# Optimization experiments

Hardware: AMD Instinct MI355X
Metric: run time of the kernel (lower is better)

Reference implementation:

```python
import jax, jax.numpy as jnp
import numpy as np


def _quant8(w):
    # Brevitas Int8 per-tensor weight quant: scale = max|w|/127, round, clip, dequant.
    s = jnp.max(jnp.abs(w)) / 127.0
    q = jnp.clip(jnp.round(w / s), -127.0, 127.0) * s
    # straight-through estimator (matches brevitas backward)
    return w + jax.lax.stop_gradient(q - w)


def _conv1d(x, w, b):
    # x: [B, Cin, L], w: [Cout, Cin, K]
    y = jax.lax.conv_general_dilated(x, w, window_strides=(1,), padding='VALID',
                                     dimension_numbers=('NCW', 'OIW', 'NCW'))
    return y + b[None, :, None]


def _maxpool2(x):
    B, C, L = x.shape
    L2 = L // 2
    return jnp.max(x[:, :, :2 * L2].reshape(B, C, L2, 2), axis=-1)


def _lrelu(x):
    return jnp.where(x > 0, x, 0.1 * x)


def setup_inputs() -> dict:
    key = jax.random.key(0)
    ks = jax.random.split(key, 13)
    B, C, L = 32768, 2, 128
    flat = 32 * 27  # 864, from tracing conv/pool stack at L=128
    d = {
        'x': jax.random.normal(ks[0], (B, C, L), dtype=jnp.float32),
        'w1': jax.random.normal(ks[1], (16, 2, 2), dtype=jnp.float32) * 0.3,
        'b1': jax.random.normal(ks[2], (16,), dtype=jnp.float32) * 0.05,
        'w2': jax.random.normal(ks[3], (16, 16, 3), dtype=jnp.float32) * 0.1,
        'b2': jax.random.normal(ks[4], (16,), dtype=jnp.float32) * 0.05,
        'w3': jax.random.normal(ks[5], (32, 16, 5), dtype=jnp.float32) * 0.1,
        'b3': jax.random.normal(ks[6], (32,), dtype=jnp.float32) * 0.05,
        'w4': jax.random.normal(ks[7], (32, 32, 5), dtype=jnp.float32) * 0.08,
        'b4': jax.random.normal(ks[8], (32,), dtype=jnp.float32) * 0.05,
        'wd': jax.random.normal(ks[9], (64, flat), dtype=jnp.float32) * 0.03,
        'bd': jax.random.normal(ks[10], (64,), dtype=jnp.float32) * 0.05,
        'wo': jax.random.normal(ks[11], (1, 64), dtype=jnp.float32) * 0.1,
        'bo': jax.random.normal(ks[12], (1,), dtype=jnp.float32) * 0.05,
    }
    return d


def reference(x, w1, b1, w2, b2, w3, b3, w4, b4, wd, bd, wo, bo):
    h = _lrelu(_conv1d(x, _quant8(w1), b1))        # [B,16,127]
    h = _lrelu(_conv1d(h, _quant8(w2), b2))        # [B,16,125]
    h = _maxpool2(h)                               # [B,16,62]
    h = _lrelu(_conv1d(h, _quant8(w3), b3))        # [B,32,58]
    h = _lrelu(_conv1d(h, _quant8(w4), b4))        # [B,32,54]
    h = _maxpool2(h)                               # [B,32,27]
    h = h.reshape(h.shape[0], -1)                  # [B,864]
    h = _lrelu(h @ _quant8(wd).T + bd)             # [B,64]
    return h @ _quant8(wo).T + bo                  # [B,1]
```

## Files before the change

### kernel.cpp

```cpp
#include <hip/hip_runtime.h>
#include <hip/hip_bf16.h>

typedef __hip_bfloat16 bf16;
typedef _Float16 h16;
typedef __attribute__((ext_vector_type(8))) _Float16 h16x8;
typedef __attribute__((ext_vector_type(4))) float f32x4;
typedef __attribute__((ext_vector_type(16))) float f32x16;

__device__ __forceinline__ float lrelu(float x) { return fmaxf(x, 0.1f * x); }
__device__ __forceinline__ float ldE(const void* p, long i, int f32) {
    return f32 ? ((const float*)p)[i] : __bfloat162float(((const bf16*)p)[i]);
}
__device__ __forceinline__ uint2 pack4(float a, float b, float c, float d) {
    union { _Float16 h[4]; uint2 u; } t;
    t.h[0] = (_Float16)a; t.h[1] = (_Float16)b; t.h[2] = (_Float16)c; t.h[3] = (_Float16)d;
    return t.u;
}
__device__ __forceinline__ unsigned umx(unsigned a, unsigned b) { return a > b ? a : b; }
#define LDS_FENCE() asm volatile("s_waitcnt lgkmcnt(0)" ::: "memory")


__device__ __forceinline__ float qv(const void* src, int idx, float sc, int f32) {
    float w = ldE(src, idx, f32);
    float q = rintf(w / sc);
    return fminf(127.f, fmaxf(-127.f, q)) * sc;
}

__device__ float block_scale(const void* src, int n, int f32, int tid, float* red) {
    unsigned m = 0;
    const uint4* p = (const uint4*)src;
    if (f32) {
        int nv = n >> 2;
        for (int i = tid; i < nv; i += 256) {
            uint4 u = p[i];
            m = umx(m, u.x & 0x7FFFFFFFu); m = umx(m, u.y & 0x7FFFFFFFu);
            m = umx(m, u.z & 0x7FFFFFFFu); m = umx(m, u.w & 0x7FFFFFFFu);
        }
        union { unsigned u; float f; } c; c.u = m;
        red[tid] = c.f;
    } else {
        int nv = n >> 3;
        for (int i = tid; i < nv; i += 256) {
            uint4 u = p[i];
            unsigned a;
            a = u.x & 0x7FFF7FFFu; m = umx(m, a >> 16); m = umx(m, a & 0xFFFFu);
            a = u.y & 0x7FFF7FFFu; m = umx(m, a >> 16); m = umx(m, a & 0xFFFFu);
            a = u.z & 0x7FFF7FFFu; m = umx(m, a >> 16); m = umx(m, a & 0xFFFFu);
            a = u.w & 0x7FFF7FFFu; m = umx(m, a >> 16); m = umx(m, a & 0xFFFFu);
        }
        union { unsigned u; float f; } c; c.u = m << 16;
        red[tid] = c.f;
    }
    __syncthreads();
    for (int s = 128; s > 0; s >>= 1) {
        if (tid < s) red[tid] = fmaxf(red[tid], red[tid + s]);
        __syncthreads();
    }
    return red[0] / 127.f;
}

__global__ void __launch_bounds__(256) prep(
    const unsigned short* __restrict__ xu,
    const void* __restrict__ w1, const void* __restrict__ w2,
    const void* __restrict__ w3, const void* __restrict__ w4,
    const void* __restrict__ wd, const void* __restrict__ wo,
    const void* __restrict__ b1, const void* __restrict__ b2,
    const void* __restrict__ b3, const void* __restrict__ b4,
    const void* __restrict__ bd, const void* __restrict__ bo,
    float* __restrict__ wsf)
{
    int tid = threadIdx.x, which = blockIdx.x;
    __shared__ float red[256];
    __shared__ int cnt;
    if (tid == 0) cnt = 0;
    __syncthreads();
    int bad = 0;
    for (int i = tid; i < 2048; i += 256) {
        int e = (xu[i] >> 7) & 0xFF;
        if (e >= 147) bad = 1;
    }
    atomicAdd(&cnt, bad);
    __syncthreads();
    const int f32 = (cnt > 4) ? 1 : 0;
    h16* wh = (h16*)(wsf + 292);

    if (which < 48) {
        float sc = block_scale(wd, 55296, f32, tid, red);
        int e1 = (which + 1) * 1152;
        for (int e = which * 1152 + tid; e < e1; e += 256) {
            int j = e & 7, l = (e >> 3) & 63, t = e >> 9;
            int mt = t / 27, c = t - mt * 27;
            int o = mt * 16 + (l & 15);
            int k = c * 32 + ((l >> 4) & 3) * 8 + j;
            int i = k >> 5, cch = k & 31;
            wh[8704 + e] = (h16)qv(wd, o * 864 + cch * 27 + i, sc, f32);
        }
    } else if (which == 48) {
        float sc = block_scale(w1, 64, f32, tid, red);
        for (int e = tid; e < 512; e += 256) {
            int l = e >> 3, j = e & 7;
            int co = l & 15, kg = (l >> 4) & 3;
            float v = (kg < 2 && j < 2) ? qv(w1, co * 4 + j * 2 + kg, sc, f32) : 0.f;
            wh[64000 + e] = (h16)v;
        }
    } else if (which == 49) {
        float sc = block_scale(w2, 768, f32, tid, red);
        for (int e = tid; e < 1024; e += 256) {
            int c = e >> 9, l = (e >> 3) & 63, j = e & 7;
            int mm = l & 15;
            int k = c * 32 + ((l >> 4) & 3) * 8 + j;
            int dk = k >> 4, ci = k & 15;
            float v = (dk < 3) ? qv(w2, (mm * 16 + ci) * 3 + dk, sc, f32) : 0.f;
            wh[0 + e] = (h16)v;
        }
    } else if (which < 52) {
        float sc = block_scale(w3, 2560, f32, tid, red);
        int e0 = (which - 50) * 1280;
        for (int e = e0 + tid; e < e0 + 1280; e += 256) {
            int c = e >> 9, l = (e >> 3) & 63, j = e & 7;
            int mm = l & 31;
            int ci = ((l >> 5) & 1) * 8 + j;
            wh[1024 + e] = (h16)qv(w3, (mm * 16 + ci) * 5 + c, sc, f32);
        }
    } else if (which < 56) {
        float sc = block_scale(w4, 5120, f32, tid, red);
        int e0 = (which - 52) * 1280;
        for (int e = e0 + tid; e < e0 + 1280; e += 256) {
            int c = e >> 9, l = (e >> 3) & 63, j = e & 7;
            int mm = l & 31;
            int k = c * 16 + ((l >> 5) & 1) * 8 + j;
            int dk = k >> 5, ci = k & 31;
            wh[3584 + e] = (h16)qv(w4, (mm * 32 + ci) * 5 + dk, sc, f32);
        }
    } else {
        float sc = block_scale(wo, 64, f32, tid, red);
        if (tid < 64) wsf[224 + tid] = qv(wo, tid, sc, f32);
        if (tid < 16)        wsf[64 + tid]        = ldE(b1, tid, f32);
        else if (tid < 32)   wsf[80 + tid - 16]   = ldE(b2, tid - 16, f32);
        else if (tid < 64)   wsf[96 + tid - 32]   = ldE(b3, tid - 32, f32);
        else if (tid < 96)   wsf[128 + tid - 64]  = ldE(b4, tid - 64, f32);
        else if (tid < 160)  wsf[160 + tid - 96]  = ldE(bd, tid - 96, f32);
        else if (tid == 160) wsf[288]             = ldE(bo, 0, f32);
        if (tid == 0) ((int*)wsf)[290] = f32;
    }
}

__global__ void __launch_bounds__(256, 2) qcnn_main(
    const void* __restrict__ x,
    const float* __restrict__ wsf,
    void* __restrict__ out)
{
    const int f32flag = ((const int*)wsf)[290];
    const h16*  wh  = (const h16*)(wsf + 292);
    const h16*  F2g = wh;
    const h16*  F3g = wh + 1024;
    const h16*  F4g = wh + 3584;
    const h16*  FDg = wh + 8704;
    const h16*  F1g = wh + 64000;

    __shared__ __align__(16) h16 Uall[4][2112];
    __shared__ __align__(16) h16 Vall[4][2208];
    __shared__ __align__(16) h16 flatb[8][872];
    __shared__ float red[256];

    int tid  = threadIdx.x;
    int lane = tid & 63;
    int w    = __builtin_amdgcn_readfirstlane(tid >> 6);
    int n16  = lane & 15, kg16 = (lane >> 4) & 3;
    int n32  = lane & 31, kg32 = (lane >> 5) & 1;
    int o16  = kg16 * 4;
    h16* U = Uall[w];
    h16* V = Vall[w];
    long b0 = (long)blockIdx.x * 8;

    h16x8 a1, a2[2], a3[5], a4[10];
    a1 = *(const h16x8*)&F1g[lane * 8];
#pragma unroll
    for (int c = 0; c < 2; ++c)  a2[c] = *(const h16x8*)&F2g[c * 512 + lane * 8];
#pragma unroll
    for (int c = 0; c < 5; ++c)  a3[c] = *(const h16x8*)&F3g[c * 512 + lane * 8];
#pragma unroll
    for (int c = 0; c < 10; ++c) a4[c] = *(const h16x8*)&F4g[c * 512 + lane * 8];
    f32x4 b1v = *(const f32x4*)&wsf[64 + o16];
    f32x4 b2v = *(const f32x4*)&wsf[80 + o16];

    const h16 hz = (h16)0.f;
    const h16x8 zrow = {hz, hz, hz, hz, hz, hz, hz, hz};

    for (int it = 0; it < 2; ++it) {
        int slot = w * 2 + it;
        long sb = (b0 + slot) * 256;

        LDS_FENCE();
        {
            float x00 = ldE(x, sb + lane, f32flag);
            float x10 = ldE(x, sb + 128 + lane, f32flag);
            float x01 = ldE(x, sb + 64 + lane, f32flag);
            float x11 = ldE(x, sb + 192 + lane, f32flag);
            h16x8 r0 = zrow, r1 = zrow;
            r0[0] = (h16)x00; r0[1] = (h16)x10;
            r1[0] = (h16)x01; r1[1] = (h16)x11;
            *(h16x8*)&V[lane * 8]        = r0;
            *(h16x8*)&V[(64 + lane) * 8] = r1;
            if (lane < 3) *(h16x8*)&V[(128 + lane) * 8] = zrow;
        }
        LDS_FENCE();

#pragma unroll
        for (int t = 0; t < 8; ++t) {
            int n = t * 16 + n16;
            f32x4 acc = b1v;
            h16x8 bfr = *(const h16x8*)&V[(n + kg16) * 8];
            acc = __builtin_amdgcn_mfma_f32_16x16x32_f16(a1, bfr, acc, 0, 0, 0);
            if (n < 127) {
                uint2 p = pack4(lrelu(acc[0]), lrelu(acc[1]), lrelu(acc[2]), lrelu(acc[3]));
                *(uint2*)&U[(o16 >> 3) * 1056 + n * 8 + (o16 & 7)] = p;
            }
        }
        if (lane < 8) {
            int g = lane & 1, row = 127 + (lane >> 1);
            *(uint4*)&U[g * 1056 + row * 8] = make_uint4(0, 0, 0, 0);
        }
        LDS_FENCE();

#pragma unroll
        for (int t = 0; t < 8; ++t) {
            int n = t * 16 + n16;
            f32x4 acc = b2v;
#pragma unroll
            for (int c = 0; c < 2; ++c) {
                int k0 = c * 32 + kg16 * 8;
                int dk = k0 >> 4, g = (k0 & 15) >> 3;
                h16x8 bfr = *(const h16x8*)&U[g * 1056 + (n + dk) * 8];
                acc = __builtin_amdgcn_mfma_f32_16x16x32_f16(a2[c], bfr, acc, 0, 0, 0);
            }
            if (n < 125) {
                uint2 p = pack4(lrelu(acc[0]), lrelu(acc[1]), lrelu(acc[2]), lrelu(acc[3]));
                *(uint2*)&V[(o16 >> 3) * 1008 + n * 8 + (o16 & 7)] = p;
            }
        }
        LDS_FENCE();

        if (lane < 62) {
#pragma unroll
            for (int g = 0; g < 2; ++g) {
                h16x8 pa = *(const h16x8*)&V[g * 1008 + (2 * lane) * 8];
                h16x8 pb = *(const h16x8*)&V[g * 1008 + (2 * lane + 1) * 8];
                h16x8 mm;
#pragma unroll
                for (int e = 0; e < 8; ++e) mm[e] = pa[e] > pb[e] ? pa[e] : pb[e];
                *(h16x8*)&U[g * 1056 + lane * 8] = mm;
            }
        }
        LDS_FENCE();

#pragma unroll
        for (int t = 0; t < 2; ++t) {
            int n = t * 32 + n32;
            f32x16 acc = {0.f,0.f,0.f,0.f,0.f,0.f,0.f,0.f,0.f,0.f,0.f,0.f,0.f,0.f,0.f,0.f};
#pragma unroll
            for (int c = 0; c < 5; ++c) {
                h16x8 bfr = *(const h16x8*)&U[kg32 * 1056 + (n + c) * 8];
                acc = __builtin_amdgcn_mfma_f32_32x32x16_f16(a3[c], bfr, acc, 0, 0, 0);
            }
            if (n < 58) {
#pragma unroll
                for (int g = 0; g < 4; ++g) {
                    int r0 = 8 * g + 4 * kg32;
                    f32x4 bv = *(const f32x4*)&wsf[96 + r0];
                    uint2 p = pack4(lrelu(acc[4*g+0] + bv[0]), lrelu(acc[4*g+1] + bv[1]),
                                    lrelu(acc[4*g+2] + bv[2]), lrelu(acc[4*g+3] + bv[3]));
                    *(uint2*)&V[g * 552 + n * 8 + 4 * kg32] = p;
                }
            }
        }
        LDS_FENCE();

#pragma unroll
        for (int t = 0; t < 2; ++t) {
            int n = t * 32 + n32;
            f32x16 acc = {0.f,0.f,0.f,0.f,0.f,0.f,0.f,0.f,0.f,0.f,0.f,0.f,0.f,0.f,0.f,0.f};
#pragma unroll
            for (int c = 0; c < 10; ++c) {
                int k0 = c * 16 + kg32 * 8;
                int dk = k0 >> 5, g = (k0 >> 3) & 3;
                h16x8 bfr = *(const h16x8*)&V[g * 552 + (n + dk) * 8];
                acc = __builtin_amdgcn_mfma_f32_32x32x16_f16(a4[c], bfr, acc, 0, 0, 0);
            }
            if (n < 54) {
#pragma unroll
                for (int g = 0; g < 4; ++g) {
                    int r0 = 8 * g + 4 * kg32;
                    f32x4 bv = *(const f32x4*)&wsf[128 + r0];
                    uint2 p = pack4(lrelu(acc[4*g+0] + bv[0]), lrelu(acc[4*g+1] + bv[1]),
                                    lrelu(acc[4*g+2] + bv[2]), lrelu(acc[4*g+3] + bv[3]));
                    *(uint2*)&U[g * 448 + n * 8 + 4 * kg32] = p;
                }
            }
        }
        LDS_FENCE();

        if (lane < 27) {
#pragma unroll
            for (int g = 0; g < 4; ++g) {
                h16x8 pa = *(const h16x8*)&U[g * 448 + (2 * lane) * 8];
                h16x8 pb = *(const h16x8*)&U[g * 448 + (2 * lane + 1) * 8];
                h16x8 mm;
#pragma unroll
                for (int e = 0; e < 8; ++e) mm[e] = pa[e] > pb[e] ? pa[e] : pb[e];
                *(h16x8*)&flatb[slot][(g * 27 + lane) * 8] = mm;
            }
        }
    }
    __syncthreads();

    int o0g = w * 16 + o16;
    f32x4 dacc = *(const f32x4*)&wsf[160 + o0g];
    for (int c = 0; c < 27; ++c) {
        h16x8 aw = *(const h16x8*)&FDg[((w * 27 + c) * 64 + lane) * 8];
        h16x8 bh = *(const h16x8*)&flatb[lane & 7][(kg16 * 27 + c) * 8];
        dacc = __builtin_amdgcn_mfma_f32_16x16x32_f16(aw, bh, dacc, 0, 0, 0);
    }
    f32x4 qov = *(const f32x4*)&wsf[224 + o0g];
    float part = 0.f;
#pragma unroll
    for (int q = 0; q < 4; ++q) part += lrelu(dacc[q]) * qov[q];
    red[tid] = part;
    __syncthreads();
    if (tid < 8) {
        float y = wsf[288];
#pragma unroll
        for (int g = 0; g < 16; ++g) y += red[(g >> 2) * 64 + (g & 3) * 16 + tid];
        if (f32flag) ((float*)out)[b0 + tid] = y;
        else         ((bf16*)out)[b0 + tid] = __float2bfloat16(y);
    }
}

extern "C" void kernel_launch(void* const* d_in, const int* in_sizes, int n_in,
                              void* d_out, int out_size, void* d_ws, size_t ws_size,
                              hipStream_t stream) {
    const void* x  = d_in[0];
    const void* w1 = d_in[1];
    const void* b1 = d_in[2];
    const void* w2 = d_in[3];
    const void* b2 = d_in[4];
    const void* w3 = d_in[5];
    const void* b3 = d_in[6];
    const void* w4 = d_in[7];
    const void* b4 = d_in[8];
    const void* wd = d_in[9];
    const void* bd = d_in[10];
    const void* wo = d_in[11];
    const void* bo = d_in[12];
    float* wsf = (float*)d_ws;

    int B = in_sizes[0] / 256;
    prep<<<57, 256, 0, stream>>>((const unsigned short*)x,
                                 w1, w2, w3, w4, wd, wo,
                                 b1, b2, b3, b4, bd, bo, wsf);
    qcnn_main<<<B / 8, 256, 0, stream>>>(x, wsf, d_out);
}
```

Baseline: 196.5 us.

## Fuse maxpool into conv epilogues via lane shuffles and split weight prep

Both maxpool stages are now computed in the conv2 and conv4 epilogues by taking a max with the neighbouring lane through __shfl_xor. The pooled values go straight into the next layer's buffer, so the intermediate LDS round-trip, one fence and the separate pooling loops per stage are gone. The prep kernel is split in two. A single-block kernel computes all six weight scales once, instead of each of the 48 wd blocks redoing the full max reduction. A second kernel then does the quantize-and-shuffle. This adds one extra kernel launch, and the single-block scale pass runs serially over about 64K weights.

```diff
diff --git a/kernel.cpp b/kernel.cpp
--- a/kernel.cpp
+++ b/kernel.cpp
@@ -56,10 +56,12 @@
         if (tid < s) red[tid] = fmaxf(red[tid], red[tid + s]);
         __syncthreads();
     }
-    return red[0] / 127.f;
-}
-
-__global__ void __launch_bounds__(256) prep(
+    float r = red[0] / 127.f;
+    __syncthreads();
+    return r;
+}
+
+__global__ void __launch_bounds__(256) prep_scales(
     const unsigned short* __restrict__ xu,
     const void* __restrict__ w1, const void* __restrict__ w2,
     const void* __restrict__ w3, const void* __restrict__ w4,
@@ -69,7 +71,7 @@
     const void* __restrict__ bd, const void* __restrict__ bo,
     float* __restrict__ wsf)
 {
-    int tid = threadIdx.x, which = blockIdx.x;
+    int tid = threadIdx.x;
     __shared__ float red[256];
     __shared__ int cnt;
     if (tid == 0) cnt = 0;
@@ -82,10 +84,40 @@
     atomicAdd(&cnt, bad);
     __syncthreads();
     const int f32 = (cnt > 4) ? 1 : 0;
-    h16* wh = (h16*)(wsf + 292);
+
+    float s1 = block_scale(w1, 64, f32, tid, red);
+    float s2 = block_scale(w2, 768, f32, tid, red);
+    float s3 = block_scale(w3, 2560, f32, tid, red);
+    float s4 = block_scale(w4, 5120, f32, tid, red);
+    float sd = block_scale(wd, 55296, f32, tid, red);
+    float so = block_scale(wo, 64, f32, tid, red);
+
+    if (tid < 64) wsf[224 + tid] = qv(wo, tid, so, f32);
+    if (tid < 16)        wsf[64 + tid]        = ldE(b1, tid, f32);
+    else if (tid < 32)   wsf[80 + tid - 16]   = ldE(b2, tid - 16, f32);
+    else if (tid < 64)   wsf[96 + tid - 32]   = ldE(b3, tid - 32, f32);
+    else if (tid < 96)   wsf[128 + tid - 64]  = ldE(b4, tid - 64, f32);
+    else if (tid < 160)  wsf[160 + tid - 96]  = ldE(bd, tid - 96, f32);
+    else if (tid == 160) wsf[288]             = ldE(bo, 0, f32);
+    if (tid == 0) {
+        ((int*)wsf)[290] = f32;
+        wsf[296] = s1; wsf[297] = s2; wsf[298] = s3;
+        wsf[299] = s4; wsf[300] = sd; wsf[301] = so;
+    }
+}
+
+__global__ void __launch_bounds__(256) prep_shuffle(
+    const void* __restrict__ w1, const void* __restrict__ w2,
+    const void* __restrict__ w3, const void* __restrict__ w4,
+    const void* __restrict__ wd,
+    float* __restrict__ wsf)
+{
+    int tid = threadIdx.x, which = blockIdx.x;
+    const int f32 = ((const int*)wsf)[290];
+    h16* wh = (h16*)(wsf + 304);
 
     if (which < 48) {
-        float sc = block_scale(wd, 55296, f32, tid, red);
+        float sc = wsf[300];
         int e1 = (which + 1) * 1152;
         for (int e = which * 1152 + tid; e < e1; e += 256) {
             int j = e & 7, l = (e >> 3) & 63, t = e >> 9;
@@ -96,7 +128,7 @@
             wh[8704 + e] = (h16)qv(wd, o * 864 + cch * 27 + i, sc, f32);
         }
     } else if (which == 48) {
-        float sc = block_scale(w1, 64, f32, tid, red);
+        float sc = wsf[296];
         for (int e = tid; e < 512; e += 256) {
             int l = e >> 3, j = e & 7;
             int co = l & 15, kg = (l >> 4) & 3;
@@ -104,7 +136,7 @@
             wh[64000 + e] = (h16)v;
         }
     } else if (which == 49) {
-        float sc = block_scale(w2, 768, f32, tid, red);
+        float sc = wsf[297];
         for (int e = tid; e < 1024; e += 256) {
             int c = e >> 9, l = (e >> 3) & 63, j = e & 7;
             int mm = l & 15;
@@ -114,7 +146,7 @@
             wh[0 + e] = (h16)v;
         }
     } else if (which < 52) {
-        float sc = block_scale(w3, 2560, f32, tid, red);
+        float sc = wsf[298];
         int e0 = (which - 50) * 1280;
         for (int e = e0 + tid; e < e0 + 1280; e += 256) {
             int c = e >> 9, l = (e >> 3) & 63, j = e & 7;
@@ -122,8 +154,8 @@
             int ci = ((l >> 5) & 1) * 8 + j;
             wh[1024 + e] = (h16)qv(w3, (mm * 16 + ci) * 5 + c, sc, f32);
         }
-    } else if (which < 56) {
-        float sc = block_scale(w4, 5120, f32, tid, red);
+    } else {
+        float sc = wsf[299];
         int e0 = (which - 52) * 1280;
         for (int e = e0 + tid; e < e0 + 1280; e += 256) {
             int c = e >> 9, l = (e >> 3) & 63, j = e & 7;
@@ -132,16 +164,6 @@
             int dk = k >> 5, ci = k & 31;
             wh[3584 + e] = (h16)qv(w4, (mm * 32 + ci) * 5 + dk, sc, f32);
         }
-    } else {
-        float sc = block_scale(wo, 64, f32, tid, red);
-        if (tid < 64) wsf[224 + tid] = qv(wo, tid, sc, f32);
-        if (tid < 16)        wsf[64 + tid]        = ldE(b1, tid, f32);
-        else if (tid < 32)   wsf[80 + tid - 16]   = ldE(b2, tid - 16, f32);
-        else if (tid < 64)   wsf[96 + tid - 32]   = ldE(b3, tid - 32, f32);
-        else if (tid < 96)   wsf[128 + tid - 64]  = ldE(b4, tid - 64, f32);
-        else if (tid < 160)  wsf[160 + tid - 96]  = ldE(bd, tid - 96, f32);
-        else if (tid == 160) wsf[288]             = ldE(bo, 0, f32);
-        if (tid == 0) ((int*)wsf)[290] = f32;
     }
 }
 
@@ -151,7 +173,7 @@
     void* __restrict__ out)
 {
     const int f32flag = ((const int*)wsf)[290];
-    const h16*  wh  = (const h16*)(wsf + 292);
+    const h16*  wh  = (const h16*)(wsf + 304);
     const h16*  F2g = wh;
     const h16*  F3g = wh + 1024;
     const h16*  F4g = wh + 3584;
@@ -234,22 +256,16 @@
                 h16x8 bfr = *(const h16x8*)&U[g * 1056 + (n + dk) * 8];
                 acc = __builtin_amdgcn_mfma_f32_16x16x32_f16(a2[c], bfr, acc, 0, 0, 0);
             }
-            if (n < 125) {
-                uint2 p = pack4(lrelu(acc[0]), lrelu(acc[1]), lrelu(acc[2]), lrelu(acc[3]));
-                *(uint2*)&V[(o16 >> 3) * 1008 + n * 8 + (o16 & 7)] = p;
-            }
-        }
-        LDS_FENCE();
-
-        if (lane < 62) {
-#pragma unroll
-            for (int g = 0; g < 2; ++g) {
-                h16x8 pa = *(const h16x8*)&V[g * 1008 + (2 * lane) * 8];
-                h16x8 pb = *(const h16x8*)&V[g * 1008 + (2 * lane + 1) * 8];
-                h16x8 mm;
-#pragma unroll
-                for (int e = 0; e < 8; ++e) mm[e] = pa[e] > pb[e] ? pa[e] : pb[e];
-                *(h16x8*)&U[g * 1056 + lane * 8] = mm;
+            float v0 = lrelu(acc[0]), v1 = lrelu(acc[1]);
+            float v2 = lrelu(acc[2]), v3 = lrelu(acc[3]);
+            v0 = fmaxf(v0, __shfl_xor(v0, 1, 64));
+            v1 = fmaxf(v1, __shfl_xor(v1, 1, 64));
+            v2 = fmaxf(v2, __shfl_xor(v2, 1, 64));
+            v3 = fmaxf(v3, __shfl_xor(v3, 1, 64));
+            if (!(n16 & 1)) {
+                int p = t * 8 + (n16 >> 1);
+                if (p < 62)
+                    *(uint2*)&U[(o16 >> 3) * 1056 + p * 8 + (o16 & 7)] = pack4(v0, v1, v2, v3);
             }
         }
         LDS_FENCE();
@@ -278,37 +294,31 @@
 
 #pragma unroll
         for (int t = 0; t < 2; ++t) {
-            int n = t * 32 + n32;
+            int n32_ = n32;  (void)n32_;
             f32x16 acc = {0.f,0.f,0.f,0.f,0.f,0.f,0.f,0.f,0.f,0.f,0.f,0.f,0.f,0.f,0.f,0.f};
 #pragma unroll
             for (int c = 0; c < 10; ++c) {
                 int k0 = c * 16 + kg32 * 8;
                 int dk = k0 >> 5, g = (k0 >> 3) & 3;
-                h16x8 bfr = *(const h16x8*)&V[g * 552 + (n + dk) * 8];
+                h16x8 bfr = *(const h16x8*)&V[g * 552 + (t * 32 + n32 + dk) * 8];
                 acc = __builtin_amdgcn_mfma_f32_32x32x16_f16(a4[c], bfr, acc, 0, 0, 0);
             }
-            if (n < 54) {
-#pragma unroll
-                for (int g = 0; g < 4; ++g) {
-                    int r0 = 8 * g + 4 * kg32;
-                    f32x4 bv = *(const f32x4*)&wsf[128 + r0];
-                    uint2 p = pack4(lrelu(acc[4*g+0] + bv[0]), lrelu(acc[4*g+1] + bv[1]),
-                                    lrelu(acc[4*g+2] + bv[2]), lrelu(acc[4*g+3] + bv[3]));
-                    *(uint2*)&U[g * 448 + n * 8 + 4 * kg32] = p;
+#pragma unroll
+            for (int g = 0; g < 4; ++g) {
+                f32x4 bv = *(const f32x4*)&wsf[128 + 8 * g + 4 * kg32];
+                float m0 = lrelu(acc[4*g+0] + bv[0]);
+                float m1 = lrelu(acc[4*g+1] + bv[1]);
+                float m2 = lrelu(acc[4*g+2] + bv[2]);
+                float m3 = lrelu(acc[4*g+3] + bv[3]);
+                m0 = fmaxf(m0, __shfl_xor(m0, 1, 64));
+                m1 = fmaxf(m1, __shfl_xor(m1, 1, 64));
+                m2 = fmaxf(m2, __shfl_xor(m2, 1, 64));
+                m3 = fmaxf(m3, __shfl_xor(m3, 1, 64));
+                if (!(n32 & 1)) {
+                    int fp = t * 16 + (n32 >> 1);
+                    if (fp < 27)
+                        *(uint2*)&flatb[slot][(g * 27 + fp) * 8 + 4 * kg32] = pack4(m0, m1, m2, m3);
                 }
-            }
-        }
-        LDS_FENCE();
-
-        if (lane < 27) {
-#pragma unroll
-            for (int g = 0; g < 4; ++g) {
-                h16x8 pa = *(const h16x8*)&U[g * 448 + (2 * lane) * 8];
-                h16x8 pb = *(const h16x8*)&U[g * 448 + (2 * lane + 1) * 8];
-                h16x8 mm;
-#pragma unroll
-                for (int e = 0; e < 8; ++e) mm[e] = pa[e] > pb[e] ? pa[e] : pb[e];
-                *(h16x8*)&flatb[slot][(g * 27 + lane) * 8] = mm;
             }
         }
     }
@@ -355,8 +365,9 @@
     float* wsf = (float*)d_ws;
 
     int B = in_sizes[0] / 256;
-    prep<<<57, 256, 0, stream>>>((const unsigned short*)x,
-                                 w1, w2, w3, w4, wd, wo,
-                                 b1, b2, b3, b4, bd, bo, wsf);
+    prep_scales<<<1, 256, 0, stream>>>((const unsigned short*)x,
+                                       w1, w2, w3, w4, wd, wo,
+                                       b1, b2, b3, b4, bd, bo, wsf);
+    prep_shuffle<<<56, 256, 0, stream>>>(w1, w2, w3, w4, wd, wsf);
     qcnn_main<<<B / 8, 256, 0, stream>>>(x, wsf, d_out);
 }
```

Result: slower. 220.2 us (+12.1%).
